# Performance work log

Measured on AMD Instinct MI355X. Metric: run time of the kernel, lower is better.

The kernel has to match this reference:

```python
import jax, jax.numpy as jnp
import numpy as np

ALPHA = 0.25
GAMMA = 2.0
W_CLASS = 2.0
W_BBOX = 5.0
W_GIOU = 2.0
EPS_LOG = 1e-8
EPS_DIV = 1e-6


def box_cxcywh_to_xyxy(b):
    cx, cy, w, h = b[..., 0], b[..., 1], b[..., 2], b[..., 3]
    return jnp.stack([cx - 0.5 * w, cy - 0.5 * h, cx + 0.5 * w, cy + 0.5 * h], axis=-1)


def generalized_box_iou(b1, b2):
    # b1: [N,4], b2: [M,4], xyxy -> giou [N,M]
    area1 = (b1[:, 2] - b1[:, 0]) * (b1[:, 3] - b1[:, 1])
    area2 = (b2[:, 2] - b2[:, 0]) * (b2[:, 3] - b2[:, 1])
    lt = jnp.maximum(b1[:, None, :2], b2[None, :, :2])
    rb = jnp.minimum(b1[:, None, 2:], b2[None, :, 2:])
    wh = jnp.maximum(rb - lt, 0.0)
    inter = wh[..., 0] * wh[..., 1]
    union = area1[:, None] + area2[None, :] - inter
    iou = inter / jnp.maximum(union, EPS_DIV)
    lt_e = jnp.minimum(b1[:, None, :2], b2[None, :, :2])
    rb_e = jnp.maximum(b1[:, None, 2:], b2[None, :, 2:])
    wh_e = jnp.maximum(rb_e - lt_e, 0.0)
    enclosing = wh_e[..., 0] * wh_e[..., 1]
    return iou - (enclosing - union) / jnp.maximum(enclosing, EPS_DIV)


def setup_inputs() -> dict:
    key = jax.random.key(0)
    k1, k2, k3, k4 = jax.random.split(key, 4)
    B, Q, C, T = 16, 900, 91, 4800  # T = 16 images * 300 targets
    pred_logits = jax.random.normal(k1, (B, Q, C), dtype=jnp.float32)
    pred_boxes = jax.random.uniform(k2, (B, Q, 4), dtype=jnp.float32)  # cxcywh in [0,1]
    tgt_ids = jax.random.randint(k3, (T,), 1, C + 1)  # 1-based labels (code uses tgt_ids - 1)
    tgt_boxes = jax.random.uniform(k4, (T, 4), dtype=jnp.float32)
    return {"pred_logits": pred_logits, "pred_boxes": pred_boxes,
            "tgt_ids": tgt_ids, "tgt_boxes": tgt_boxes}


def reference(pred_logits, pred_boxes, tgt_ids, tgt_boxes):
    B, Q, C = pred_logits.shape
    pl = jax.nn.sigmoid(pred_logits.reshape(B * Q, C))   # [BQ, C]
    pb = pred_boxes.reshape(B * Q, 4)                    # [BQ, 4]

    # focal-style class cost
    neg_cost = (1.0 - ALPHA) * pl ** GAMMA * (-jnp.log(1.0 - pl + EPS_LOG))
    pos_cost = ALPHA * (1.0 - pl) ** GAMMA * (-jnp.log(pl + EPS_LOG))
    cost_class = (pos_cost - neg_cost)[:, tgt_ids - 1]   # [BQ, T]

    # L1 box cost (cdist, p=1)
    cost_bbox = jnp.sum(jnp.abs(pb[:, None, :] - tgt_boxes[None, :, :]), axis=-1)  # [BQ, T]

    # negative generalized IoU cost
    cost_giou = -generalized_box_iou(box_cxcywh_to_xyxy(pb), box_cxcywh_to_xyxy(tgt_boxes))

    Cmat = W_CLASS * cost_class + W_BBOX * cost_bbox + W_GIOU * cost_giou
    return Cmat.reshape(B, Q, -1)  # [B, Q, T]
```

## Files before the change

### kernel.cpp

```cpp
#include <hip/hip_runtime.h>

constexpr int kB = 16, kQ = 900, kC = 91, kT = 4800;
constexpr int kBQ = kB * kQ;
constexpr int kTI = 16;

__global__ __launch_bounds__(256)
void class_cost_kernel(const float* __restrict__ logits,
                       float* __restrict__ cd, int n) {
    int idx = blockIdx.x * 256 + threadIdx.x;
    if (idx >= n) return;
    float x = logits[idx];
    float p = 1.0f / (1.0f + expf(-x));
    float omp = 1.0f - p;
    float pos = 0.25f * omp * omp * (-logf(p + 1e-8f));
    float neg = 0.75f * p * p * (-logf(omp + 1e-8f));
    cd[idx] = 2.0f * (pos - neg);
}

__global__ __launch_bounds__(256)
void cost_kernel(const float* __restrict__ pred_boxes,
                 const int*   __restrict__ tgt_ids,
                 const float* __restrict__ tgt_boxes,
                 const float* __restrict__ cd,
                 float*       __restrict__ out) {
    const int j  = blockIdx.x * 256 + threadIdx.x;
    const int i0 = blockIdx.y * kTI;
    const bool valid = (j < kT);

    float tcx = 0.f, tcy = 0.f, tw = 0.f, th = 0.f;
    float tx0 = 0.f, ty0 = 0.f, tx1 = 0.f, ty1 = 0.f, ta = 0.f;
    int tc = 0;
    if (valid) {
        float4 tb = reinterpret_cast<const float4*>(tgt_boxes)[j];
        tcx = tb.x; tcy = tb.y; tw = tb.z; th = tb.w;
        tx0 = tcx - 0.5f * tw;  ty0 = tcy - 0.5f * th;
        tx1 = tcx + 0.5f * tw;  ty1 = tcy + 0.5f * th;
        ta  = tw * th;
        tc  = tgt_ids[j] - 1;
    }

    for (int ii = 0; ii < kTI; ++ii) {
        const int i = i0 + ii;
        float4 pb = reinterpret_cast<const float4*>(pred_boxes)[i];
        float pcx = pb.x, pcy = pb.y, pw = pb.z, ph = pb.w;
        float px0 = pcx - 0.5f * pw, py0 = pcy - 0.5f * ph;
        float px1 = pcx + 0.5f * pw, py1 = pcy + 0.5f * ph;
        float pa  = pw * ph;

        float cdv = valid ? cd[i * kC + tc] : 0.f;

        float l1 = fabsf(pcx - tcx) + fabsf(pcy - tcy)
                 + fabsf(pw  - tw ) + fabsf(ph  - th );

        float lx = fmaxf(px0, tx0), ly = fmaxf(py0, ty0);
        float rx = fminf(px1, tx1), ry = fminf(py1, ty1);
        float iw = fmaxf(rx - lx, 0.f), ih = fmaxf(ry - ly, 0.f);
        float inter = iw * ih;
        float uni   = pa + ta - inter;
        float iou   = inter * __builtin_amdgcn_rcpf(fmaxf(uni, 1e-6f));

        float ex0 = fminf(px0, tx0), ey0 = fminf(py0, ty0);
        float ex1 = fmaxf(px1, tx1), ey1 = fmaxf(py1, ty1);
        float ew  = fmaxf(ex1 - ex0, 0.f), eh = fmaxf(ey1 - ey0, 0.f);
        float enc = ew * eh;
        float giou = iou - (enc - uni) * __builtin_amdgcn_rcpf(fmaxf(enc, 1e-6f));

        float cost = cdv + 5.0f * l1 - 2.0f * giou;

        if (valid) out[(size_t)i * kT + j] = cost;
    }
}

extern "C" void kernel_launch(void* const* d_in, const int* in_sizes, int n_in,
                              void* d_out, int out_size, void* d_ws, size_t ws_size,
                              hipStream_t stream) {
    const float* logits  = (const float*)d_in[0];
    const float* pboxes  = (const float*)d_in[1];
    const int*   tids    = (const int*)d_in[2];
    const float* tboxes  = (const float*)d_in[3];
    float* out = (float*)d_out;
    float* cd  = (float*)d_ws;

    const int n_cd = kBQ * kC;
    class_cost_kernel<<<(n_cd + 255) / 256, 256, 0, stream>>>(logits, cd, n_cd);

    dim3 grid((kT + 255) / 256, kBQ / kTI);
    cost_kernel<<<grid, 256, 0, stream>>>(pboxes, tids, tboxes, cd, out);
}
```

Measured before the change: 329.2 us.

## Stage class costs and pred boxes in LDS, compute 4 targets per thread

The cost kernel now stages the 16 rows of class costs and predicted boxes for its block in shared memory, so the per-element gather reads from LDS instead of global memory. Each thread handles four consecutive targets and writes them with one float4 store. The grid shrinks by a factor of four in x. With kT=4800 and 1024 targets per block, the fifth x-block has threads that are partly out of range; these skip their work through the valid check. Fewer blocks in x and more registers per thread could lower occupancy.

```diff
diff --git a/kernel.cpp b/kernel.cpp
--- a/kernel.cpp
+++ b/kernel.cpp
@@ -3,6 +3,9 @@
 constexpr int kB = 16, kQ = 900, kC = 91, kT = 4800;
 constexpr int kBQ = kB * kQ;
 constexpr int kTI = 16;
+constexpr int kJT = 4;
+constexpr int kBT = 256;
+constexpr int kJB = kBT * kJT;
 
 __global__ __launch_bounds__(256)
 void class_cost_kernel(const float* __restrict__ logits,
@@ -23,51 +26,79 @@
                  const float* __restrict__ tgt_boxes,
                  const float* __restrict__ cd,
                  float*       __restrict__ out) {
-    const int j  = blockIdx.x * 256 + threadIdx.x;
-    const int i0 = blockIdx.y * kTI;
-    const bool valid = (j < kT);
+    __shared__ float  lds_cd[kTI * kC];
+    __shared__ float4 lds_pb[kTI];
 
-    float tcx = 0.f, tcy = 0.f, tw = 0.f, th = 0.f;
-    float tx0 = 0.f, ty0 = 0.f, tx1 = 0.f, ty1 = 0.f, ta = 0.f;
-    int tc = 0;
+    const int tid = threadIdx.x;
+    const int i0  = blockIdx.y * kTI;
+    const int j0  = blockIdx.x * kJB + tid * kJT;
+    const bool valid = (j0 + kJT <= kT);
+
+    for (int k = tid; k < kTI * kC; k += kBT)
+        lds_cd[k] = cd[i0 * kC + k];
+    if (tid < kTI)
+        lds_pb[tid] = reinterpret_cast<const float4*>(pred_boxes)[i0 + tid];
+    __syncthreads();
+
+    float tcx[kJT], tcy[kJT], tw[kJT], th[kJT];
+    float tx0[kJT], ty0[kJT], tx1[kJT], ty1[kJT], ta[kJT];
+    int   tco[kJT];
     if (valid) {
-        float4 tb = reinterpret_cast<const float4*>(tgt_boxes)[j];
-        tcx = tb.x; tcy = tb.y; tw = tb.z; th = tb.w;
-        tx0 = tcx - 0.5f * tw;  ty0 = tcy - 0.5f * th;
-        tx1 = tcx + 0.5f * tw;  ty1 = tcy + 0.5f * th;
-        ta  = tw * th;
-        tc  = tgt_ids[j] - 1;
+        int4 ids = *reinterpret_cast<const int4*>(&tgt_ids[j0]);
+        tco[0] = ids.x - 1; tco[1] = ids.y - 1; tco[2] = ids.z - 1; tco[3] = ids.w - 1;
+        #pragma unroll
+        for (int q = 0; q < kJT; ++q) {
+            float4 tb = reinterpret_cast<const float4*>(tgt_boxes)[j0 + q];
+            tcx[q] = tb.x; tcy[q] = tb.y; tw[q] = tb.z; th[q] = tb.w;
+            tx0[q] = tb.x - 0.5f * tb.z;  ty0[q] = tb.y - 0.5f * tb.w;
+            tx1[q] = tb.x + 0.5f * tb.z;  ty1[q] = tb.y + 0.5f * tb.w;
+            ta[q]  = tb.z * tb.w;
+        }
+    } else {
+        #pragma unroll
+        for (int q = 0; q < kJT; ++q) {
+            tcx[q] = tcy[q] = tw[q] = th[q] = 0.f;
+            tx0[q] = ty0[q] = tx1[q] = ty1[q] = ta[q] = 0.f;
+            tco[q] = 0;
+        }
     }
 
     for (int ii = 0; ii < kTI; ++ii) {
-        const int i = i0 + ii;
-        float4 pb = reinterpret_cast<const float4*>(pred_boxes)[i];
-        float pcx = pb.x, pcy = pb.y, pw = pb.z, ph = pb.w;
-        float px0 = pcx - 0.5f * pw, py0 = pcy - 0.5f * ph;
-        float px1 = pcx + 0.5f * pw, py1 = pcy + 0.5f * ph;
-        float pa  = pw * ph;
+        const float4 pb = lds_pb[ii];
+        const float pcx = pb.x, pcy = pb.y, pw = pb.z, ph = pb.w;
+        const float px0 = pcx - 0.5f * pw, py0 = pcy - 0.5f * ph;
+        const float px1 = pcx + 0.5f * pw, py1 = pcy + 0.5f * ph;
+        const float pa  = pw * ph;
 
-        float cdv = valid ? cd[i * kC + tc] : 0.f;
+        float4 res;
+        #pragma unroll
+        for (int q = 0; q < kJT; ++q) {
+            float cdv = lds_cd[ii * kC + tco[q]];
 
-        float l1 = fabsf(pcx - tcx) + fabsf(pcy - tcy)
-                 + fabsf(pw  - tw ) + fabsf(ph  - th );
+            float l1 = fabsf(pcx - tcx[q]) + fabsf(pcy - tcy[q])
+                     + fabsf(pw  - tw[q] ) + fabsf(ph  - th[q] );
 
-        float lx = fmaxf(px0, tx0), ly = fmaxf(py0, ty0);
-        float rx = fminf(px1, tx1), ry = fminf(py1, ty1);
-        float iw = fmaxf(rx - lx, 0.f), ih = fmaxf(ry - ly, 0.f);
-        float inter = iw * ih;
-        float uni   = pa + ta - inter;
-        float iou   = inter * __builtin_amdgcn_rcpf(fmaxf(uni, 1e-6f));
+            float lx = fmaxf(px0, tx0[q]), ly = fmaxf(py0, ty0[q]);
+            float rx = fminf(px1, tx1[q]), ry = fminf(py1, ty1[q]);
+            float iw = fmaxf(rx - lx, 0.f), ih = fmaxf(ry - ly, 0.f);
+            float inter = iw * ih;
+            float uni   = pa + ta[q] - inter;
+            float iou   = inter * __builtin_amdgcn_rcpf(fmaxf(uni, 1e-6f));
 
-        float ex0 = fminf(px0, tx0), ey0 = fminf(py0, ty0);
-        float ex1 = fmaxf(px1, tx1), ey1 = fmaxf(py1, ty1);
-        float ew  = fmaxf(ex1 - ex0, 0.f), eh = fmaxf(ey1 - ey0, 0.f);
-        float enc = ew * eh;
-        float giou = iou - (enc - uni) * __builtin_amdgcn_rcpf(fmaxf(enc, 1e-6f));
+            float ex0 = fminf(px0, tx0[q]), ey0 = fminf(py0, ty0[q]);
+            float ex1 = fmaxf(px1, tx1[q]), ey1 = fmaxf(py1, ty1[q]);
+            float ew  = fmaxf(ex1 - ex0, 0.f), eh = fmaxf(ey1 - ey0, 0.f);
+            float enc = ew * eh;
+            float giou = iou - (enc - uni) * __builtin_amdgcn_rcpf(fmaxf(enc, 1e-6f));
 
-        float cost = cdv + 5.0f * l1 - 2.0f * giou;
+            float c = cdv + 5.0f * l1 - 2.0f * giou;
+            (&res.x)[q] = c;
+        }
 
-        if (valid) out[(size_t)i * kT + j] = cost;
+        if (valid) {
+            size_t off = (size_t)(i0 + ii) * kT + j0;
+            *reinterpret_cast<float4*>(&out[off]) = res;
+        }
     }
 }
 
@@ -84,6 +115,6 @@
     const int n_cd = kBQ * kC;
     class_cost_kernel<<<(n_cd + 255) / 256, 256, 0, stream>>>(logits, cd, n_cd);
 
-    dim3 grid((kT + 255) / 256, kBQ / kTI);
+    dim3 grid((kT + kJB - 1) / kJB, kBQ / kTI);
     cost_kernel<<<grid, 256, 0, stream>>>(pboxes, tids, tboxes, cd, out);
 }
```

New measurement: 316.0 us. -4.0%, faster.
